# Kernel optimization log

Measured on AMD Instinct MI355X. Metric: run time of the kernel, lower is better.

Reference implementation:

```python
import jax, jax.numpy as jnp
import numpy as np
from jax import lax

NUM_VARS = 16384
NUM_CHECKS = 8192
BATCH = 32
MAX_ITER = 15
H_DENSITY = 0.001  # ~8 ones per column, LDPC-like Tanner graph


def setup_inputs() -> dict:
    key = jax.random.key(0)
    k_h, k_s, k_l = jax.random.split(key, 3)
    # Sparse binary parity-check matrix represented densely (same math).
    parity_matrix = (jax.random.uniform(k_h, (NUM_CHECKS, NUM_VARS)) < H_DENSITY).astype(jnp.float32)
    syndrome = jax.random.randint(k_s, (BATCH, NUM_CHECKS), 0, 2).astype(jnp.float32)
    channel_llrs = jax.random.normal(k_l, (BATCH, NUM_VARS), dtype=jnp.float32)
    w_vc = jnp.ones((1,), dtype=jnp.float32)
    w_cv = jnp.ones((1,), dtype=jnp.float32)
    damping = jnp.float32(0.5)
    return {
        "syndrome": syndrome,
        "parity_matrix": parity_matrix,
        "channel_llrs": channel_llrs,
        "w_vc": w_vc,
        "w_cv": w_cv,
        "damping": damping,
    }


def reference(syndrome, parity_matrix, channel_llrs, w_vc, w_cv, damping):
    # syndrome: (B, C); parity_matrix H: (C, V); channel_llrs: (B, V)
    s_sign = 1.0 - 2.0 * syndrome  # (B, C)

    def body(v_beliefs, _):
        # v -> c: sparse.mm(H, v^T)^T == v @ H^T  -> (B, C)
        v_to_c = w_vc * (v_beliefs @ parity_matrix.T)
        c_msg = s_sign * jnp.tanh(v_to_c * 0.5)  # (B, C)
        # c -> v: sparse.mm(H^T, c^T)^T == c @ H  -> (B, V)
        c_to_v = w_cv * (c_msg @ parity_matrix)
        v_new = damping * v_beliefs + (1.0 - damping) * (channel_llrs + c_to_v)
        return v_new, None

    v_beliefs, _ = lax.scan(body, channel_llrs, None, length=MAX_ITER)
    return jax.nn.sigmoid(-v_beliefs)  # (B, V) bit-flip probabilities
```

## Files before the change

kernel.cpp:

```cpp
#include <hip/hip_runtime.h>


#define C_NUM 8192
#define V_NUM 16384
#define B_NUM 32
#define RW 64
#define CW 32

#define RQ 12
#define CQ 8
#define RQ_S 13
#define CQ_S 9

#define NBLK 256
#define NTHR 1024
#define NTH (NBLK * NTHR)

#define WCAP 256

#define BEL_SL (16400 * 4)
#define CMS_SL (8200 * 4)

typedef unsigned short u16;
typedef unsigned int u32;
typedef unsigned long long u64;

#define ZERO_WORDS ((C_NUM + V_NUM))
#define NBAR 32
#define BAR_STRIDE 64

__device__ __forceinline__ float agent_ldf(const float* p) {
    return __hip_atomic_load(p, __ATOMIC_RELAXED, __HIP_MEMORY_SCOPE_AGENT);
}
__device__ __forceinline__ void agent_stf(float* p, float v) {
    __hip_atomic_store(p, v, __ATOMIC_RELAXED, __HIP_MEMORY_SCOPE_AGENT);
}
__device__ __forceinline__ u64 agent_ld64(const u64* p) {
    return __hip_atomic_load(p, __ATOMIC_RELAXED, __HIP_MEMORY_SCOPE_AGENT);
}
__device__ __forceinline__ int agent_ldi(const int* p) {
    return __hip_atomic_load(p, __ATOMIC_RELAXED, __HIP_MEMORY_SCOPE_AGENT);
}
__device__ __forceinline__ void agent_st32(u32* p, u32 v) {
    __hip_atomic_store(p, v, __ATOMIC_RELAXED, __HIP_MEMORY_SCOPE_AGENT);
}
__device__ __forceinline__ void agent_st16(u16* p, u16 v) {
    __hip_atomic_store(p, v, __ATOMIC_RELAXED, __HIP_MEMORY_SCOPE_AGENT);
}

__device__ __forceinline__ void grid_barrier(u32* bars, int id) {
    __syncthreads();
    if (threadIdx.x == 0) {
        u32* base = bars + id * 8 * BAR_STRIDE;
        asm volatile("s_waitcnt vmcnt(0) lgkmcnt(0)" ::: "memory");
        __hip_atomic_fetch_add(base + (blockIdx.x & 7) * BAR_STRIDE, 1u,
                               __ATOMIC_RELAXED, __HIP_MEMORY_SCOPE_AGENT);
        u32 sum;
        do {
            sum = 0;
#pragma unroll
            for (int g = 0; g < 8; ++g)
                sum += __hip_atomic_load(base + g * BAR_STRIDE,
                                         __ATOMIC_RELAXED, __HIP_MEMORY_SCOPE_AGENT);
            if (sum < (u32)NBLK) __builtin_amdgcn_s_sleep(4);
        } while (sum < (u32)NBLK);
        asm volatile("" ::: "memory");
    }
    __syncthreads();
}

__device__ __forceinline__ float fast_tanh_half(float x) {
    float ax = fabsf(x);
    float e = __expf(-ax);
    return copysignf((1.0f - e) / (1.0f + e), x);
}

template<bool LOCAL>
__device__ __forceinline__ void ld4(const float* p0, const float* p1,
                                    const float* p2, const float* p3,
                                    float& r0, float& r1, float& r2, float& r3) {
    if (LOCAL) {
        asm volatile(
            "global_load_dword %0, %4, off sc0\n\t"
            "global_load_dword %1, %5, off sc0\n\t"
            "global_load_dword %2, %6, off sc0\n\t"
            "global_load_dword %3, %7, off sc0\n\t"
            "s_waitcnt vmcnt(0)"
            : "=&v"(r0), "=&v"(r1), "=&v"(r2), "=&v"(r3)
            : "v"(p0), "v"(p1), "v"(p2), "v"(p3)
            : "memory");
    } else {
        r0 = agent_ldf(p0); r1 = agent_ldf(p1);
        r2 = agent_ldf(p2); r3 = agent_ldf(p3);
    }
}

template<bool LOCAL>
__device__ __forceinline__ void decode_tail(
    int G, int R,
    const float* __restrict__ synd, const float* __restrict__ llr,
    const int* __restrict__ row_cnt, const int* __restrict__ col_cnt,
    const u16* __restrict__ row_idx, const u16* __restrict__ col_idx,
    float* __restrict__ bel_x, float* __restrict__ cms_x,
    u32* __restrict__ bars, float* __restrict__ out,
    u64* ls_row, u64* ls_col,
    float wvc, float wcv, float d)
{
    const int t = threadIdx.x;
    const int b4 = t & 3;
    const int qid = t >> 2;
    float* const belS = bel_x + (size_t)G * BEL_SL;
    float* const cmsS = cms_x + (size_t)G * CMS_SL;

    for (int e = t; e < 256 * RQ; e += NTHR) {
        int rl = e / RQ, p = e - rl * RQ;
        int c = (R << 8) + rl;
        int n = agent_ldi(&row_cnt[c]); n = n > 4 * RQ ? 4 * RQ : n;
        u64 q = agent_ld64(&((const u64*)(row_idx + (size_t)c * RW))[p]);
        int j = 4 * p;
        u64 a0 = (j + 0 < n) ? (q & 0xFFFFu) : (u64)V_NUM;
        u64 a1 = (j + 1 < n) ? ((q >> 16) & 0xFFFFu) : (u64)V_NUM;
        u64 a2 = (j + 2 < n) ? ((q >> 32) & 0xFFFFu) : (u64)V_NUM;
        u64 a3 = (j + 3 < n) ? (q >> 48) : (u64)V_NUM;
        ls_row[rl * RQ_S + p] = a0 | (a1 << 16) | (a2 << 32) | (a3 << 48);
    }
    for (int e = t; e < 512 * CQ; e += NTHR) {
        int gl = e >> 3, p = e & 7;
        int v = (gl < 256) ? ((R << 8) + gl) : (C_NUM + (R << 8) + (gl - 256));
        int n = agent_ldi(&col_cnt[v]); n = n > 4 * CQ ? 4 * CQ : n;
        u64 q = agent_ld64(&((const u64*)(col_idx + (size_t)v * CW))[p]);
        int j = 4 * p;
        u64 a0 = (j + 0 < n) ? (q & 0xFFFFu) : (u64)C_NUM;
        u64 a1 = (j + 1 < n) ? ((q >> 16) & 0xFFFFu) : (u64)C_NUM;
        u64 a2 = (j + 2 < n) ? ((q >> 32) & 0xFFFFu) : (u64)C_NUM;
        u64 a3 = (j + 3 < n) ? (q >> 48) : (u64)C_NUM;
        ls_col[gl * CQ_S + p] = a0 | (a1 << 16) | (a2 << 32) | (a3 << 48);
    }
    const int c_my = (R << 8) + qid;
    const int v0_my = (R << 8) + qid;
    const int v1_my = C_NUM + (R << 8) + qid;
    int nrow;  { int n = agent_ldi(&row_cnt[c_my]);  nrow  = n > 4*RQ ? 4*RQ : n; }
    int ncol0; { int n = agent_ldi(&col_cnt[v0_my]); ncol0 = n > 4*CQ ? 4*CQ : n; }
    int ncol1; { int n = agent_ldi(&col_cnt[v1_my]); ncol1 = n > 4*CQ ? 4*CQ : n; }
    const int b = (G << 2) + b4;
    const float ss = 1.0f - 2.0f * synd[b * C_NUM + c_my];
    const float llr0 = llr[b * V_NUM + v0_my];
    const float llr1 = llr[b * V_NUM + v1_my];
    float bel0 = llr0, bel1 = llr1;
    if (LOCAL) {
        belS[v0_my * 4 + b4] = bel0;
        belS[v1_my * 4 + b4] = bel1;
    } else {
        agent_stf(&belS[v0_my * 4 + b4], bel0);
        agent_stf(&belS[v1_my * 4 + b4], bel1);
    }

    grid_barrier(bars, 2);

    const u64* const rowL  = ls_row + qid * RQ_S;
    const u64* const colL0 = ls_col + qid * CQ_S;
    const u64* const colL1 = ls_col + (256 + qid) * CQ_S;
    float* const cms_own  = cmsS + c_my * 4 + b4;
    float* const bel_own0 = belS + v0_my * 4 + b4;
    float* const bel_own1 = belS + v1_my * 4 + b4;

    int barid = 3;
    for (int it = 0; it < 15; ++it) {
        {
            float sum = 0.0f;
#pragma unroll
            for (int p = 0; p < RQ; ++p) {
                if (4 * p < nrow) {
                    u64 q = rowL[p];
                    const float* a0 = belS + (int)(q & 0xFFFFu) * 4 + b4;
                    const float* a1 = belS + (int)((q >> 16) & 0xFFFFu) * 4 + b4;
                    const float* a2 = belS + (int)((q >> 32) & 0xFFFFu) * 4 + b4;
                    const float* a3 = belS + (int)(q >> 48) * 4 + b4;
                    float s0, s1, s2, s3;
                    ld4<LOCAL>(a0, a1, a2, a3, s0, s1, s2, s3);
                    sum += s0; sum += s1; sum += s2; sum += s3;
                }
            }
            float m = ss * fast_tanh_half(wvc * sum);
            if (LOCAL) *cms_own = m; else agent_stf(cms_own, m);
        }
        grid_barrier(bars, barid++);

        bool last = (it == 14);
        float sum0 = 0.0f, sum1 = 0.0f;
#pragma unroll
        for (int p = 0; p < CQ; ++p) {
            if (4 * p < ncol0) {
                u64 q = colL0[p];
                const float* a0 = cmsS + (int)(q & 0xFFFFu) * 4 + b4;
                const float* a1 = cmsS + (int)((q >> 16) & 0xFFFFu) * 4 + b4;
                const float* a2 = cmsS + (int)((q >> 32) & 0xFFFFu) * 4 + b4;
                const float* a3 = cmsS + (int)(q >> 48) * 4 + b4;
                float s0, s1, s2, s3;
                ld4<LOCAL>(a0, a1, a2, a3, s0, s1, s2, s3);
                sum0 += s0; sum0 += s1; sum0 += s2; sum0 += s3;
            }
        }
#pragma unroll
        for (int p = 0; p < CQ; ++p) {
            if (4 * p < ncol1) {
                u64 q = colL1[p];
                const float* a0 = cmsS + (int)(q & 0xFFFFu) * 4 + b4;
                const float* a1 = cmsS + (int)((q >> 16) & 0xFFFFu) * 4 + b4;
                const float* a2 = cmsS + (int)((q >> 32) & 0xFFFFu) * 4 + b4;
                const float* a3 = cmsS + (int)(q >> 48) * 4 + b4;
                float s0, s1, s2, s3;
                ld4<LOCAL>(a0, a1, a2, a3, s0, s1, s2, s3);
                sum1 += s0; sum1 += s1; sum1 += s2; sum1 += s3;
            }
        }
        float nb0 = d * bel0 + (1.0f - d) * (llr0 + wcv * sum0);
        float nb1 = d * bel1 + (1.0f - d) * (llr1 + wcv * sum1);
        bel0 = nb0; bel1 = nb1;
        if (!last) {
            if (LOCAL) { *bel_own0 = nb0; *bel_own1 = nb1; }
            else { agent_stf(bel_own0, nb0); agent_stf(bel_own1, nb1); }
            grid_barrier(bars, barid++);
        } else {
            out[b * V_NUM + v0_my] = 1.0f / (1.0f + __expf(nb0));
            out[b * V_NUM + v1_my] = 1.0f / (1.0f + __expf(nb1));
        }
    }
}

__global__ __launch_bounds__(NTHR, 1)
void bp_fused(const float* __restrict__ H,
              const float* __restrict__ synd,
              const float* __restrict__ llr,
              const float* __restrict__ w_vc_p,
              const float* __restrict__ w_cv_p,
              const float* __restrict__ damp_p,
              int* __restrict__ row_cnt, int* __restrict__ col_cnt,
              u16* __restrict__ row_idx, u16* __restrict__ col_idx,
              float* __restrict__ bel_x, float* __restrict__ cms_x,
              u32* __restrict__ bars, int* __restrict__ xcd_cnt,
              float* __restrict__ out) {
    const int tid = blockIdx.x * NTHR + threadIdx.x;
    const int lane = threadIdx.x & 63;

    __shared__ u32 lds_edges[(NTHR / 64) * WCAP + 1024];
    __shared__ u64 ls_row[256 * RQ_S];
    __shared__ u64 ls_col[512 * CQ_S];
    __shared__ int s_xcd, s_rank;
    u32* const wl = lds_edges + (threadIdx.x >> 6) * WCAP;

    if (threadIdx.x == 0) {
        u32 x;
        asm volatile("s_getreg_b32 %0, hwreg(HW_REG_XCC_ID)" : "=s"(x));
        x &= 15;
        s_xcd = (int)x;
        s_rank = atomicAdd(&xcd_cnt[x], 1);
    }

    {
        u32* zp = (u32*)row_cnt;
        for (int t = tid; t < ZERO_WORDS; t += NTH) agent_st32(&zp[t], 0u);
        if (tid < 32) {
            int g = tid >> 2, j = tid & 3;
            agent_stf(&bel_x[(size_t)g * BEL_SL + V_NUM * 4 + j], 0.0f);
        } else if (tid < 64) {
            int g = (tid - 32) >> 2, j = tid & 3;
            agent_stf(&cms_x[(size_t)g * CMS_SL + C_NUM * 4 + j], 0.0f);
        }
    }

    int wave_cnt;
    {
        const float4* Hv = (const float4*)H;
        const u64 ltmask = (1ull << lane) - 1ull;
        int wb = 0;
        int ta = tid;
        int tb = tid + 2 * NTH;
        float4 a0 = Hv[ta], a1 = Hv[ta + NTH];
        float4 b0 = Hv[tb], b1 = Hv[tb + NTH];
#pragma unroll 1
        for (int itn = 0; itn < 64; ++itn) {
            int tc = tb + 2 * NTH;
            float4 p0, p1;
            if (itn < 62) { p0 = Hv[tc]; p1 = Hv[tc + NTH]; }
            float vals[8] = {a0.x, a0.y, a0.z, a0.w, a1.x, a1.y, a1.z, a1.w};
#pragma unroll
            for (int k = 0; k < 8; ++k) {
                bool nz = vals[k] != 0.0f;
                u64 bb = __ballot(nz);
                if (bb) {
                    if (nz) {
                        int ee = (k < 4) ? (ta * 4 + k)
                                         : ((ta + NTH) * 4 + (k - 4));
                        int off = wb + (int)__popcll(bb & ltmask);
                        if (off < WCAP) wl[off] = (u32)ee;
                    }
                    wb += (int)__popcll(bb);
                }
            }
            a0 = b0; a1 = b1; b0 = p0; b1 = p1; ta = tb; tb = tc;
        }
        wave_cnt = wb < WCAP ? wb : WCAP;
    }
    grid_barrier(bars, 0);

    {
        for (int e = lane; e < wave_cnt; e += 64) {
            u32 ee = wl[e];
            int c = (int)(ee >> 14);
            int v = (int)(ee & (V_NUM - 1));
            int rs = atomicAdd(&row_cnt[c], 1);
            if (rs < RW) agent_st16(&row_idx[(size_t)c * RW + rs], (u16)v);
            int cs = atomicAdd(&col_cnt[v], 1);
            if (cs < CW) agent_st16(&col_idx[(size_t)v * CW + cs], (u16)c);
        }
    }
    grid_barrier(bars, 1);

    int my_xcd = s_xcd, my_rank = s_rank;
    bool balanced = true;
#pragma unroll
    for (int g = 0; g < 8; ++g) balanced &= (agent_ldi(&xcd_cnt[g]) == 32);

    const float wvc = w_vc_p[0];
    const float wcv = w_cv_p[0];
    const float d   = damp_p[0];

    if (balanced) {
        decode_tail<true>(my_xcd, my_rank, synd, llr, row_cnt, col_cnt,
                          row_idx, col_idx, bel_x, cms_x, bars, out,
                          ls_row, ls_col, wvc, wcv, d);
    } else {
        decode_tail<false>((int)(blockIdx.x >> 5), (int)(blockIdx.x & 31),
                           synd, llr, row_cnt, col_cnt,
                           row_idx, col_idx, bel_x, cms_x, bars, out,
                           ls_row, ls_col, wvc, wcv, d);
    }
}

extern "C" void kernel_launch(void* const* d_in, const int* in_sizes, int n_in,
                              void* d_out, int out_size, void* d_ws, size_t ws_size,
                              hipStream_t stream) {
    const float* synd = (const float*)d_in[0];
    const float* H    = (const float*)d_in[1];
    const float* llr  = (const float*)d_in[2];
    const float* w_vc = (const float*)d_in[3];
    const float* w_cv = (const float*)d_in[4];
    const float* damp = (const float*)d_in[5];
    float* out = (float*)d_out;

    char* ws = (char*)d_ws;
    size_t off = 0;
    int* row_cnt = (int*)(ws + off); off += (size_t)C_NUM * 4;
    int* col_cnt = (int*)(ws + off); off += (size_t)V_NUM * 4;
    u16* row_idx = (u16*)(ws + off); off += (size_t)C_NUM * RW * 2;
    u16* col_idx = (u16*)(ws + off); off += (size_t)V_NUM * CW * 2;
    float* bel_x = (float*)(ws + off); off += (size_t)8 * BEL_SL * 4;
    float* cms_x = (float*)(ws + off); off += (size_t)8 * CMS_SL * 4;
    u32* bars  = (u32*)(ws + off); off += (size_t)NBAR * 8 * BAR_STRIDE * 4;
    int* xcd_cnt = (int*)(ws + off); off += 64;

    hipMemsetAsync(bars, 0, (size_t)NBAR * 8 * BAR_STRIDE * 4 + 64, stream);

    void* args[] = {
        (void*)&H, (void*)&synd, (void*)&llr,
        (void*)&w_vc, (void*)&w_cv, (void*)&damp,
        (void*)&row_cnt, (void*)&col_cnt, (void*)&row_idx, (void*)&col_idx,
        (void*)&bel_x, (void*)&cms_x, (void*)&bars, (void*)&xcd_cnt,
        (void*)&out
    };
    hipLaunchCooperativeKernel((const void*)bp_fused,
                               dim3(NBLK), dim3(NTHR), args, 0, stream);
}
```

Measured before the change: 921.5 us.

## Split H scan into separate high-occupancy kernel and batch gathers into 16-load groups

Moves the dense parity-matrix scan and edge-list build out of the cooperative decode kernel into its own kernel with 2048 blocks of 256 threads. The scan, which reads the full 512MB matrix, then runs at much higher occupancy than the 256-block cooperative grid, and the row/column counters are zeroed with a memset. In the decode loop, gathers are now issued 16 loads at a time with wave-uniform skipping of the extra groups, giving more memory-level parallelism. The cost is an extra kernel launch plus loads of padding entries whenever any lane in a wave needs a further group.

```diff
diff --git a/kernel.cpp b/kernel.cpp
--- a/kernel.cpp
+++ b/kernel.cpp
@@ -14,7 +14,10 @@
 
 #define NBLK 256
 #define NTHR 1024
-#define NTH (NBLK * NTHR)
+
+#define NBLK_A 2048
+#define NTHR_A 256
+#define NT_A (NBLK_A * NTHR_A)
 
 #define WCAP 256
 
@@ -25,7 +28,6 @@
 typedef unsigned int u32;
 typedef unsigned long long u64;
 
-#define ZERO_WORDS ((C_NUM + V_NUM))
 #define NBAR 32
 #define BAR_STRIDE 64
 
@@ -40,9 +42,6 @@
 }
 __device__ __forceinline__ int agent_ldi(const int* p) {
     return __hip_atomic_load(p, __ATOMIC_RELAXED, __HIP_MEMORY_SCOPE_AGENT);
-}
-__device__ __forceinline__ void agent_st32(u32* p, u32 v) {
-    __hip_atomic_store(p, v, __ATOMIC_RELAXED, __HIP_MEMORY_SCOPE_AGENT);
 }
 __device__ __forceinline__ void agent_st16(u16* p, u16 v) {
     __hip_atomic_store(p, v, __ATOMIC_RELAXED, __HIP_MEMORY_SCOPE_AGENT);
@@ -76,22 +75,101 @@
 }
 
 template<bool LOCAL>
-__device__ __forceinline__ void ld4(const float* p0, const float* p1,
-                                    const float* p2, const float* p3,
-                                    float& r0, float& r1, float& r2, float& r3) {
+__device__ __forceinline__ float sum16(const float* __restrict__ base,
+                                       const u64* __restrict__ q4, int b4) {
+    const float* a[16];
+#pragma unroll
+    for (int p = 0; p < 4; ++p) {
+        u64 q = q4[p];
+        a[4 * p + 0] = base + (int)(q & 0xFFFFu) * 4 + b4;
+        a[4 * p + 1] = base + (int)((q >> 16) & 0xFFFFu) * 4 + b4;
+        a[4 * p + 2] = base + (int)((q >> 32) & 0xFFFFu) * 4 + b4;
+        a[4 * p + 3] = base + (int)(q >> 48) * 4 + b4;
+    }
+    float r[16];
     if (LOCAL) {
         asm volatile(
-            "global_load_dword %0, %4, off sc0\n\t"
-            "global_load_dword %1, %5, off sc0\n\t"
-            "global_load_dword %2, %6, off sc0\n\t"
-            "global_load_dword %3, %7, off sc0\n\t"
+            "global_load_dword %0, %16, off sc0\n\t"
+            "global_load_dword %1, %17, off sc0\n\t"
+            "global_load_dword %2, %18, off sc0\n\t"
+            "global_load_dword %3, %19, off sc0\n\t"
+            "global_load_dword %4, %20, off sc0\n\t"
+            "global_load_dword %5, %21, off sc0\n\t"
+            "global_load_dword %6, %22, off sc0\n\t"
+            "global_load_dword %7, %23, off sc0\n\t"
+            "global_load_dword %8, %24, off sc0\n\t"
+            "global_load_dword %9, %25, off sc0\n\t"
+            "global_load_dword %10, %26, off sc0\n\t"
+            "global_load_dword %11, %27, off sc0\n\t"
+            "global_load_dword %12, %28, off sc0\n\t"
+            "global_load_dword %13, %29, off sc0\n\t"
+            "global_load_dword %14, %30, off sc0\n\t"
+            "global_load_dword %15, %31, off sc0\n\t"
             "s_waitcnt vmcnt(0)"
-            : "=&v"(r0), "=&v"(r1), "=&v"(r2), "=&v"(r3)
-            : "v"(p0), "v"(p1), "v"(p2), "v"(p3)
+            : "=&v"(r[0]), "=&v"(r[1]), "=&v"(r[2]), "=&v"(r[3]),
+              "=&v"(r[4]), "=&v"(r[5]), "=&v"(r[6]), "=&v"(r[7]),
+              "=&v"(r[8]), "=&v"(r[9]), "=&v"(r[10]), "=&v"(r[11]),
+              "=&v"(r[12]), "=&v"(r[13]), "=&v"(r[14]), "=&v"(r[15])
+            : "v"(a[0]), "v"(a[1]), "v"(a[2]), "v"(a[3]),
+              "v"(a[4]), "v"(a[5]), "v"(a[6]), "v"(a[7]),
+              "v"(a[8]), "v"(a[9]), "v"(a[10]), "v"(a[11]),
+              "v"(a[12]), "v"(a[13]), "v"(a[14]), "v"(a[15])
             : "memory");
     } else {
-        r0 = agent_ldf(p0); r1 = agent_ldf(p1);
-        r2 = agent_ldf(p2); r3 = agent_ldf(p3);
+#pragma unroll
+        for (int j = 0; j < 16; ++j) r[j] = agent_ldf(a[j]);
+    }
+    float s0 = (r[0] + r[1]) + (r[2] + r[3]);
+    float s1 = (r[4] + r[5]) + (r[6] + r[7]);
+    float s2 = (r[8] + r[9]) + (r[10] + r[11]);
+    float s3 = (r[12] + r[13]) + (r[14] + r[15]);
+    return (s0 + s1) + (s2 + s3);
+}
+
+__global__ __launch_bounds__(NTHR_A, 8)
+void scan_build(const float* __restrict__ H,
+                int* __restrict__ row_cnt, int* __restrict__ col_cnt,
+                u16* __restrict__ row_idx, u16* __restrict__ col_idx) {
+    __shared__ u32 lds_edges[(NTHR_A / 64) * WCAP];
+    const int lane = threadIdx.x & 63;
+    u32* const wl = lds_edges + (threadIdx.x >> 6) * WCAP;
+    const u64 ltmask = (1ull << lane) - 1ull;
+    const float4* Hv = (const float4*)H;
+    const u32 t0 = blockIdx.x * NTHR_A + threadIdx.x;
+    int wb = 0;
+#pragma unroll 1
+    for (int i = 0; i < 8; ++i) {
+        float4 h[8];
+#pragma unroll
+        for (int k = 0; k < 8; ++k)
+            h[k] = Hv[t0 + (u32)(i * 8 + k) * (u32)NT_A];
+#pragma unroll
+        for (int k = 0; k < 8; ++k) {
+            u32 eb = (t0 + (u32)(i * 8 + k) * (u32)NT_A) * 4u;
+            float vals[4] = {h[k].x, h[k].y, h[k].z, h[k].w};
+#pragma unroll
+            for (int kk = 0; kk < 4; ++kk) {
+                bool nz = vals[kk] != 0.0f;
+                u64 bb = __ballot(nz);
+                if (bb) {
+                    if (nz) {
+                        int off = wb + (int)__popcll(bb & ltmask);
+                        if (off < WCAP) wl[off] = eb + kk;
+                    }
+                    wb += (int)__popcll(bb);
+                }
+            }
+        }
+    }
+    int wave_cnt = wb < WCAP ? wb : WCAP;
+    for (int e = lane; e < wave_cnt; e += 64) {
+        u32 ee = wl[e];
+        int c = (int)(ee >> 14);
+        int v = (int)(ee & (V_NUM - 1));
+        int rs = atomicAdd(&row_cnt[c], 1);
+        if (rs < RW) agent_st16(&row_idx[(size_t)c * RW + rs], (u16)v);
+        int cs = atomicAdd(&col_cnt[v], 1);
+        if (cs < CW) agent_st16(&col_idx[(size_t)v * CW + cs], (u16)c);
     }
 }
 
@@ -155,7 +233,7 @@
         agent_stf(&belS[v1_my * 4 + b4], bel1);
     }
 
-    grid_barrier(bars, 2);
+    grid_barrier(bars, 1);
 
     const u64* const rowL  = ls_row + qid * RQ_S;
     const u64* const colL0 = ls_col + qid * CQ_S;
@@ -164,56 +242,23 @@
     float* const bel_own0 = belS + v0_my * 4 + b4;
     float* const bel_own1 = belS + v1_my * 4 + b4;
 
-    int barid = 3;
+    int barid = 2;
     for (int it = 0; it < 15; ++it) {
         {
-            float sum = 0.0f;
-#pragma unroll
-            for (int p = 0; p < RQ; ++p) {
-                if (4 * p < nrow) {
-                    u64 q = rowL[p];
-                    const float* a0 = belS + (int)(q & 0xFFFFu) * 4 + b4;
-                    const float* a1 = belS + (int)((q >> 16) & 0xFFFFu) * 4 + b4;
-                    const float* a2 = belS + (int)((q >> 32) & 0xFFFFu) * 4 + b4;
-                    const float* a3 = belS + (int)(q >> 48) * 4 + b4;
-                    float s0, s1, s2, s3;
-                    ld4<LOCAL>(a0, a1, a2, a3, s0, s1, s2, s3);
-                    sum += s0; sum += s1; sum += s2; sum += s3;
-                }
-            }
+            float sum = sum16<LOCAL>(belS, rowL, b4);
+            if (__any(nrow > 16)) sum += sum16<LOCAL>(belS, rowL + 4, b4);
+            if (__any(nrow > 32)) sum += sum16<LOCAL>(belS, rowL + 8, b4);
             float m = ss * fast_tanh_half(wvc * sum);
             if (LOCAL) *cms_own = m; else agent_stf(cms_own, m);
         }
         grid_barrier(bars, barid++);
 
         bool last = (it == 14);
-        float sum0 = 0.0f, sum1 = 0.0f;
-#pragma unroll
-        for (int p = 0; p < CQ; ++p) {
-            if (4 * p < ncol0) {
-                u64 q = colL0[p];
-                const float* a0 = cmsS + (int)(q & 0xFFFFu) * 4 + b4;
-                const float* a1 = cmsS + (int)((q >> 16) & 0xFFFFu) * 4 + b4;
-                const float* a2 = cmsS + (int)((q >> 32) & 0xFFFFu) * 4 + b4;
-                const float* a3 = cmsS + (int)(q >> 48) * 4 + b4;
-                float s0, s1, s2, s3;
-                ld4<LOCAL>(a0, a1, a2, a3, s0, s1, s2, s3);
-                sum0 += s0; sum0 += s1; sum0 += s2; sum0 += s3;
-            }
-        }
-#pragma unroll
-        for (int p = 0; p < CQ; ++p) {
-            if (4 * p < ncol1) {
-                u64 q = colL1[p];
-                const float* a0 = cmsS + (int)(q & 0xFFFFu) * 4 + b4;
-                const float* a1 = cmsS + (int)((q >> 16) & 0xFFFFu) * 4 + b4;
-                const float* a2 = cmsS + (int)((q >> 32) & 0xFFFFu) * 4 + b4;
-                const float* a3 = cmsS + (int)(q >> 48) * 4 + b4;
-                float s0, s1, s2, s3;
-                ld4<LOCAL>(a0, a1, a2, a3, s0, s1, s2, s3);
-                sum1 += s0; sum1 += s1; sum1 += s2; sum1 += s3;
-            }
-        }
+        float sum0 = sum16<LOCAL>(cmsS, colL0, b4);
+        if (__any(ncol0 > 16)) sum0 += sum16<LOCAL>(cmsS, colL0 + 4, b4);
+        float sum1 = sum16<LOCAL>(cmsS, colL1, b4);
+        if (__any(ncol1 > 16)) sum1 += sum16<LOCAL>(cmsS, colL1 + 4, b4);
+
         float nb0 = d * bel0 + (1.0f - d) * (llr0 + wcv * sum0);
         float nb1 = d * bel1 + (1.0f - d) * (llr1 + wcv * sum1);
         bel0 = nb0; bel1 = nb1;
@@ -228,96 +273,41 @@
     }
 }
 
-__global__ __launch_bounds__(NTHR, 1)
-void bp_fused(const float* __restrict__ H,
-              const float* __restrict__ synd,
-              const float* __restrict__ llr,
-              const float* __restrict__ w_vc_p,
-              const float* __restrict__ w_cv_p,
-              const float* __restrict__ damp_p,
-              int* __restrict__ row_cnt, int* __restrict__ col_cnt,
-              u16* __restrict__ row_idx, u16* __restrict__ col_idx,
-              float* __restrict__ bel_x, float* __restrict__ cms_x,
-              u32* __restrict__ bars, int* __restrict__ xcd_cnt,
-              float* __restrict__ out) {
-    const int tid = blockIdx.x * NTHR + threadIdx.x;
-    const int lane = threadIdx.x & 63;
-
-    __shared__ u32 lds_edges[(NTHR / 64) * WCAP + 1024];
-    __shared__ u64 ls_row[256 * RQ_S];
-    __shared__ u64 ls_col[512 * CQ_S];
+__global__ __launch_bounds__(NTHR, 1) __attribute__((amdgpu_waves_per_eu(4, 4)))
+void bp_decode(const float* __restrict__ synd,
+               const float* __restrict__ llr,
+               const float* __restrict__ w_vc_p,
+               const float* __restrict__ w_cv_p,
+               const float* __restrict__ damp_p,
+               const int* __restrict__ row_cnt, const int* __restrict__ col_cnt,
+               const u16* __restrict__ row_idx, const u16* __restrict__ col_idx,
+               float* __restrict__ bel_x, float* __restrict__ cms_x,
+               u32* __restrict__ bars, int* __restrict__ xcd_cnt,
+               float* __restrict__ out) {
+    const int t = threadIdx.x;
+    const int tid = blockIdx.x * NTHR + t;
+
+    __shared__ u64 shpool[10496];
     __shared__ int s_xcd, s_rank;
-    u32* const wl = lds_edges + (threadIdx.x >> 6) * WCAP;
-
-    if (threadIdx.x == 0) {
+    u64* const ls_row = shpool;
+    u64* const ls_col = shpool + 256 * RQ_S;
+
+    if (t == 0) {
         u32 x;
         asm volatile("s_getreg_b32 %0, hwreg(HW_REG_XCC_ID)" : "=s"(x));
         x &= 15;
         s_xcd = (int)x;
         s_rank = atomicAdd(&xcd_cnt[x], 1);
     }
-
-    {
-        u32* zp = (u32*)row_cnt;
-        for (int t = tid; t < ZERO_WORDS; t += NTH) agent_st32(&zp[t], 0u);
-        if (tid < 32) {
-            int g = tid >> 2, j = tid & 3;
-            agent_stf(&bel_x[(size_t)g * BEL_SL + V_NUM * 4 + j], 0.0f);
-        } else if (tid < 64) {
-            int g = (tid - 32) >> 2, j = tid & 3;
-            agent_stf(&cms_x[(size_t)g * CMS_SL + C_NUM * 4 + j], 0.0f);
-        }
-    }
-
-    int wave_cnt;
-    {
-        const float4* Hv = (const float4*)H;
-        const u64 ltmask = (1ull << lane) - 1ull;
-        int wb = 0;
-        int ta = tid;
-        int tb = tid + 2 * NTH;
-        float4 a0 = Hv[ta], a1 = Hv[ta + NTH];
-        float4 b0 = Hv[tb], b1 = Hv[tb + NTH];
-#pragma unroll 1
-        for (int itn = 0; itn < 64; ++itn) {
-            int tc = tb + 2 * NTH;
-            float4 p0, p1;
-            if (itn < 62) { p0 = Hv[tc]; p1 = Hv[tc + NTH]; }
-            float vals[8] = {a0.x, a0.y, a0.z, a0.w, a1.x, a1.y, a1.z, a1.w};
-#pragma unroll
-            for (int k = 0; k < 8; ++k) {
-                bool nz = vals[k] != 0.0f;
-                u64 bb = __ballot(nz);
-                if (bb) {
-                    if (nz) {
-                        int ee = (k < 4) ? (ta * 4 + k)
-                                         : ((ta + NTH) * 4 + (k - 4));
-                        int off = wb + (int)__popcll(bb & ltmask);
-                        if (off < WCAP) wl[off] = (u32)ee;
-                    }
-                    wb += (int)__popcll(bb);
-                }
-            }
-            a0 = b0; a1 = b1; b0 = p0; b1 = p1; ta = tb; tb = tc;
-        }
-        wave_cnt = wb < WCAP ? wb : WCAP;
+    if (tid < 32) {
+        int g = tid >> 2, j = tid & 3;
+        agent_stf(&bel_x[(size_t)g * BEL_SL + V_NUM * 4 + j], 0.0f);
+    } else if (tid < 64) {
+        int g = (tid - 32) >> 2, j = tid & 3;
+        agent_stf(&cms_x[(size_t)g * CMS_SL + C_NUM * 4 + j], 0.0f);
     }
     grid_barrier(bars, 0);
 
-    {
-        for (int e = lane; e < wave_cnt; e += 64) {
-            u32 ee = wl[e];
-            int c = (int)(ee >> 14);
-            int v = (int)(ee & (V_NUM - 1));
-            int rs = atomicAdd(&row_cnt[c], 1);
-            if (rs < RW) agent_st16(&row_idx[(size_t)c * RW + rs], (u16)v);
-            int cs = atomicAdd(&col_cnt[v], 1);
-            if (cs < CW) agent_st16(&col_idx[(size_t)v * CW + cs], (u16)c);
-        }
-    }
-    grid_barrier(bars, 1);
-
-    int my_xcd = s_xcd, my_rank = s_rank;
     bool balanced = true;
 #pragma unroll
     for (int g = 0; g < 8; ++g) balanced &= (agent_ldi(&xcd_cnt[g]) == 32);
@@ -327,7 +317,7 @@
     const float d   = damp_p[0];
 
     if (balanced) {
-        decode_tail<true>(my_xcd, my_rank, synd, llr, row_cnt, col_cnt,
+        decode_tail<true>(s_xcd, s_rank, synd, llr, row_cnt, col_cnt,
                           row_idx, col_idx, bel_x, cms_x, bars, out,
                           ls_row, ls_col, wvc, wcv, d);
     } else {
@@ -360,15 +350,18 @@
     u32* bars  = (u32*)(ws + off); off += (size_t)NBAR * 8 * BAR_STRIDE * 4;
     int* xcd_cnt = (int*)(ws + off); off += 64;
 
+    hipMemsetAsync(row_cnt, 0, (size_t)(C_NUM + V_NUM) * 4, stream);
     hipMemsetAsync(bars, 0, (size_t)NBAR * 8 * BAR_STRIDE * 4 + 64, stream);
 
+    hipLaunchKernelGGL(scan_build, dim3(NBLK_A), dim3(NTHR_A), 0, stream,
+                       H, row_cnt, col_cnt, row_idx, col_idx);
+
     void* args[] = {
-        (void*)&H, (void*)&synd, (void*)&llr,
-        (void*)&w_vc, (void*)&w_cv, (void*)&damp,
+        (void*)&synd, (void*)&llr, (void*)&w_vc, (void*)&w_cv, (void*)&damp,
         (void*)&row_cnt, (void*)&col_cnt, (void*)&row_idx, (void*)&col_idx,
         (void*)&bel_x, (void*)&cms_x, (void*)&bars, (void*)&xcd_cnt,
         (void*)&out
     };
-    hipLaunchCooperativeKernel((const void*)bp_fused,
+    hipLaunchCooperativeKernel((const void*)bp_decode,
                                dim3(NBLK), dim3(NTHR), args, 0, stream);
 }
```

Result: slower. 947.8 us (+2.9%).
